# Kernel optimization log

Measured on AMD Instinct MI355X. Metric: run time of the kernel, lower is better.

The kernel has to match this reference:

```python
import jax, jax.numpy as jnp
import numpy as np

N = 100000
E = 1600000
C = 128
NEG_SLOPE = 0.2
BN_EPS = 1e-5


def setup_inputs() -> dict:
    key = jax.random.key(0)
    ks = jax.random.split(key, 6)
    x = jax.random.normal(ks[0], (N, C), dtype=jnp.float32)
    edge_index = jax.random.randint(ks[1], (2, E), 0, N, dtype=jnp.int64)
    # Glorot-ish scaled params, stacked over the 3 layers (all 128->128)
    Ws = jax.random.normal(ks[2], (3, C, C), dtype=jnp.float32) * (1.0 / np.sqrt(C))
    att_srcs = jax.random.normal(ks[3], (3, C), dtype=jnp.float32) * (1.0 / np.sqrt(C))
    att_dsts = jax.random.normal(ks[4], (3, C), dtype=jnp.float32) * (1.0 / np.sqrt(C))
    biases = jnp.zeros((3, C), dtype=jnp.float32)
    gammas = jnp.ones((3, C), dtype=jnp.float32)
    betas = jnp.zeros((3, C), dtype=jnp.float32)
    return {"x": x, "edge_index": edge_index, "Ws": Ws, "att_srcs": att_srcs,
            "att_dsts": att_dsts, "biases": biases, "gammas": gammas, "betas": betas}


def _gat_layer(x, W, a_src, a_dst, bias, src, dst):
    # linear transform: [N, C]
    h = x @ W
    # per-node attention logits
    s_src = h @ a_src  # [N]
    s_dst = h @ a_dst  # [N]
    # edge-wise gather + leaky relu scoring
    e = jax.nn.leaky_relu(s_src[src] + s_dst[dst], NEG_SLOPE)  # [E+N]
    # scatter-softmax over incoming edges of each target node
    m = jax.ops.segment_max(e, dst, num_segments=N)  # every node has a self-loop
    ex = jnp.exp(e - m[dst])
    denom = jax.ops.segment_sum(ex, dst, num_segments=N)
    alpha = ex / denom[dst]  # [E+N]
    # scatter-add aggregation of alpha-weighted source features
    out = jax.ops.segment_sum(alpha[:, None] * h[src], dst, num_segments=N)
    return out + bias


def _batch_norm(x, gamma, beta):
    mu = jnp.mean(x, axis=0)
    var = jnp.mean(jnp.square(x - mu), axis=0)
    return gamma * (x - mu) * jax.lax.rsqrt(var + BN_EPS) + beta


def reference(x, edge_index, Ws, att_srcs, att_dsts, biases, gammas, betas):
    # PyG GATConv adds self-loops by default
    loops = jnp.arange(N, dtype=edge_index.dtype)
    src = jnp.concatenate([edge_index[0], loops])
    dst = jnp.concatenate([edge_index[1], loops])
    outs = []
    for l in range(3):
        x = _gat_layer(x, Ws[l], att_srcs[l], att_dsts[l], biases[l], src, dst)
        x = jax.nn.relu(x)
        x = _batch_norm(x, gammas[l], betas[l])
        outs.append(x)
    # jump=True: concat all layer outputs -> [N, 3*C]
    return jnp.concatenate(outs, axis=-1)
```

## Files before the change

### kernel.cpp

```cpp
#include <hip/hip_runtime.h>
#include <math.h>

#define N_NODES 100000
#define N_EDGES 1600000
#define M_TOT   (N_EDGES + N_NODES)
#define C_DIM   128
#define NEG_SLOPE 0.2f
#define BN_EPS 1e-5f

#define NBUCK 8
#define BUCK_NODES 12500
#define BUCK_CAP 240000

#define KS2 72
#define BN_NB 256
#define SCAN_NB 98

typedef _Float16 f16x8 __attribute__((ext_vector_type(8)));
typedef float f32x4 __attribute__((ext_vector_type(4)));

static __device__ __forceinline__ unsigned short f2h(float f) {
    _Float16 h = (_Float16)f;
    unsigned short u;
    __builtin_memcpy(&u, &h, 2);
    return u;
}
static __device__ __forceinline__ float h2f(unsigned short u) {
    _Float16 h;
    __builtin_memcpy(&h, &u, 2);
    return (float)h;
}

__global__ void zero_i32(int* __restrict__ p, int n) {
    int i = blockIdx.x * blockDim.x + threadIdx.x;
    if (i < n) p[i] = 0;
}

__global__ __launch_bounds__(256) void bucket_edges(const int* __restrict__ ei,
                                                    int* __restrict__ bucket_next,
                                                    int2* __restrict__ buckets) {
    __shared__ int cnt[NBUCK];
    __shared__ int base[NBUCK];
    int tid = threadIdx.x;
    if (tid < NBUCK) cnt[tid] = 0;
    __syncthreads();
    int m = blockIdx.x * 256 + tid;
    int src = 0, dst = 0, p = 0, myoff = 0;
    bool valid = (m < M_TOT);
    if (valid) {
        if (m < N_EDGES) { src = ei[m]; dst = ei[N_EDGES + m]; }
        else             { src = m - N_EDGES; dst = src; }
        p = dst / BUCK_NODES;
        myoff = atomicAdd(&cnt[p], 1);
    }
    __syncthreads();
    if (tid < NBUCK) base[tid] = (cnt[tid] > 0) ? atomicAdd(&bucket_next[tid], cnt[tid]) : 0;
    __syncthreads();
    if (valid) {
        buckets[(size_t)p * BUCK_CAP + base[p] + myoff] = make_int2(src, dst);
    }
}

__global__ __launch_bounds__(256) void count_deg_b(const int2* __restrict__ buckets,
                                                   const int* __restrict__ bucket_next,
                                                   int* __restrict__ deg) {
    int p = blockIdx.x & 7;
    int chunk = blockIdx.x >> 3;
    int len = bucket_next[p];
    const int2* b = buckets + (size_t)p * BUCK_CAP;
    int stride = (gridDim.x >> 3) * 256;
    for (int i = chunk * 256 + threadIdx.x; i < len; i += stride) {
        atomicAdd(&deg[b[i].y], 1);
    }
}

__global__ __launch_bounds__(256) void scatter_b(const int2* __restrict__ buckets,
                                                 const int* __restrict__ bucket_next,
                                                 int* __restrict__ nextp,
                                                 int* __restrict__ csr_src) {
    int p = blockIdx.x & 7;
    int chunk = blockIdx.x >> 3;
    int len = bucket_next[p];
    const int2* b = buckets + (size_t)p * BUCK_CAP;
    int stride = (gridDim.x >> 3) * 256;
    for (int i = chunk * 256 + threadIdx.x; i < len; i += stride) {
        int2 e = b[i];
        int pos = atomicAdd(&nextp[e.y], 1);
        csr_src[pos] = e.x;
    }
}

__global__ __launch_bounds__(256) void block_sums(const int* __restrict__ deg,
                                                  int* __restrict__ partials) {
    __shared__ int lds[256];
    int base = blockIdx.x * 1024;
    int s = 0;
    for (int i = threadIdx.x; i < 1024; i += 256) {
        int idx = base + i;
        if (idx < N_NODES) s += deg[idx];
    }
    lds[threadIdx.x] = s;
    __syncthreads();
    for (int off = 128; off > 0; off >>= 1) {
        if (threadIdx.x < off) lds[threadIdx.x] += lds[threadIdx.x + off];
        __syncthreads();
    }
    if (threadIdx.x == 0) partials[blockIdx.x] = lds[0];
}

__global__ __launch_bounds__(128) void scan_partials(int* __restrict__ partials, int nb,
                                                     int* __restrict__ row_ptr) {
    __shared__ int lds[128];
    int tid = threadIdx.x;
    int v = (tid < nb) ? partials[tid] : 0;
    lds[tid] = v;
    __syncthreads();
    for (int off = 1; off < 128; off <<= 1) {
        int t = (tid >= off) ? lds[tid - off] : 0;
        __syncthreads();
        lds[tid] += t;
        __syncthreads();
    }
    if (tid < nb) partials[tid] = lds[tid] - v;
    if (tid == 0) row_ptr[N_NODES] = M_TOT;
}

__global__ __launch_bounds__(256) void scan_write(const int* __restrict__ deg,
                                                  const int* __restrict__ partials,
                                                  int* __restrict__ row_ptr,
                                                  int* __restrict__ nextp) {
    __shared__ int lds[256];
    int tid = threadIdx.x;
    int base = blockIdx.x * 1024;
    int i0 = base + tid * 4;
    int d[4];
#pragma unroll
    for (int t = 0; t < 4; ++t)
        d[t] = (i0 + t < N_NODES) ? deg[i0 + t] : 0;
    int tsum = d[0] + d[1] + d[2] + d[3];
    lds[tid] = tsum;
    __syncthreads();
    for (int off = 1; off < 256; off <<= 1) {
        int v = (tid >= off) ? lds[tid - off] : 0;
        __syncthreads();
        lds[tid] += v;
        __syncthreads();
    }
    int excl = lds[tid] - tsum;
    int run = partials[blockIdx.x] + excl;
#pragma unroll
    for (int t = 0; t < 4; ++t) {
        if (i0 + t < N_NODES) {
            row_ptr[i0 + t] = run;
            nextp[i0 + t]   = run;
            run += d[t];
        }
    }
}

__global__ __launch_bounds__(256, 3) void gemm_attn(
    const float* __restrict__ X, int ldx,
    const float* __restrict__ W,
    const float* __restrict__ a_src, const float* __restrict__ a_dst,
    unsigned short* __restrict__ Hh, float* __restrict__ Ssrc,
    float* __restrict__ Sdst) {
    __shared__ unsigned short Xs[128 * KS2];
    __shared__ unsigned short Wt[128 * KS2];
    int tid = threadIdx.x;
    int rbase = blockIdx.x * 128;

    int wave = tid >> 6;
    int lane = tid & 63;
    int q = lane >> 4;
    int l15 = lane & 15;
    int wrow = wave * 32;

    f32x4 acc[2][8] = {};

    for (int kb = 0; kb < 128; kb += 64) {
        __syncthreads();
        {
            int rl = tid >> 4;
            int cg = (tid & 15) * 4;
#pragma unroll
            for (int i = 0; i < 8; ++i) {
                int r = rl + i * 16;
                int row = rbase + r;
                if (row >= N_NODES) row = N_NODES - 1;
                float4 v = *(const float4*)&X[(size_t)row * ldx + kb + cg];
                ushort4 o;
                o.x = f2h(v.x); o.y = f2h(v.y); o.z = f2h(v.z); o.w = f2h(v.w);
                *(ushort4*)&Xs[r * KS2 + cg] = o;
            }
        }
        {
            int kl = tid >> 5;
            int n4 = (tid & 31) * 4;
#pragma unroll
            for (int i = 0; i < 8; ++i) {
                int kk = kl + i * 8;
                float4 v = *(const float4*)&W[(kb + kk) * 128 + n4];
                Wt[(n4 + 0) * KS2 + kk] = f2h(v.x);
                Wt[(n4 + 1) * KS2 + kk] = f2h(v.y);
                Wt[(n4 + 2) * KS2 + kk] = f2h(v.z);
                Wt[(n4 + 3) * KS2 + kk] = f2h(v.w);
            }
        }
        __syncthreads();
#pragma unroll
        for (int ks = 0; ks < 64; ks += 32) {
            int k0 = ks + q * 8;
            f16x8 a0 = *(f16x8*)&Xs[(wrow + l15) * KS2 + k0];
            f16x8 a1 = *(f16x8*)&Xs[(wrow + 16 + l15) * KS2 + k0];
#pragma unroll
            for (int c = 0; c < 8; ++c) {
                f16x8 b = *(f16x8*)&Wt[(c * 16 + l15) * KS2 + k0];
                acc[0][c] = __builtin_amdgcn_mfma_f32_16x16x32_f16(a0, b, acc[0][c], 0, 0, 0);
                acc[1][c] = __builtin_amdgcn_mfma_f32_16x16x32_f16(a1, b, acc[1][c], 0, 0, 0);
            }
        }
    }

    float avs[8], avd[8];
#pragma unroll
    for (int c = 0; c < 8; ++c) {
        avs[c] = a_src[c * 16 + l15];
        avd[c] = a_dst[c * 16 + l15];
    }
#pragma unroll
    for (int r = 0; r < 2; ++r) {
        float ps[4] = {0, 0, 0, 0}, pd[4] = {0, 0, 0, 0};
#pragma unroll
        for (int g = 0; g < 4; ++g) {
            int row = rbase + wrow + r * 16 + q * 4 + g;
            bool ok = (row < N_NODES);
#pragma unroll
            for (int c = 0; c < 8; ++c) {
                float h = acc[r][c][g];
                if (ok) Hh[(size_t)row * 128 + c * 16 + l15] = f2h(h);
                ps[g] = fmaf(h, avs[c], ps[g]);
                pd[g] = fmaf(h, avd[c], pd[g]);
            }
        }
#pragma unroll
        for (int g = 0; g < 4; ++g) {
#pragma unroll
            for (int off = 1; off < 16; off <<= 1) {
                ps[g] += __shfl_xor(ps[g], off, 64);
                pd[g] += __shfl_xor(pd[g], off, 64);
            }
        }
        if (l15 == 0) {
#pragma unroll
            for (int g = 0; g < 4; ++g) {
                int row = rbase + wrow + r * 16 + q * 4 + g;
                if (row < N_NODES) {
                    Ssrc[row] = ps[g];
                    Sdst[row] = pd[g];
                }
            }
        }
    }
}

__global__ __launch_bounds__(256) void aggregate(
    const unsigned short* __restrict__ Hh, const int* __restrict__ row_ptr,
    const int* __restrict__ csr_src,
    const float* __restrict__ Ssrc, const float* __restrict__ Sdst,
    const float* __restrict__ bias, float* __restrict__ Y) {
    int wave = threadIdx.x >> 6;
    int lane = threadIdx.x & 63;
    int g = lane >> 4;
    int l15 = lane & 15;
    int v = blockIdx.x * 4 + wave;
    int start = row_ptr[v];
    int end = row_ptr[v + 1];
    float sdv = Sdst[v];

    float sself = Ssrc[v] + sdv;
    float m = (sself > 0.0f) ? sself : NEG_SLOPE * sself;

    float acc[8] = {0, 0, 0, 0, 0, 0, 0, 0};
    float denom = 0.0f;

    int j = start;
    for (; j + 8 <= end; j += 8) {
        int u0 = csr_src[j + g];
        int u1 = csr_src[j + 4 + g];
        float ss0 = Ssrc[u0];
        float ss1 = Ssrc[u1];
        f16x8 h0 = *(const f16x8*)&Hh[(size_t)u0 * 128 + l15 * 8];
        f16x8 h1 = *(const f16x8*)&Hh[(size_t)u1 * 128 + l15 * 8];
        float s0 = ss0 + sdv; s0 = (s0 > 0.0f) ? s0 : NEG_SLOPE * s0;
        float s1 = ss1 + sdv; s1 = (s1 > 0.0f) ? s1 : NEG_SLOPE * s1;
        float w0 = __expf(s0 - m);
        float w1 = __expf(s1 - m);
        denom += w0 + w1;
#pragma unroll
        for (int i = 0; i < 8; ++i) acc[i] = fmaf(w0, (float)h0[i], acc[i]);
#pragma unroll
        for (int i = 0; i < 8; ++i) acc[i] = fmaf(w1, (float)h1[i], acc[i]);
    }
    for (; j < end; j += 4) {
        int je = j + g;
        bool ok = (je < end);
        int u = ok ? csr_src[je] : v;
        float s = Ssrc[u] + sdv; s = (s > 0.0f) ? s : NEG_SLOPE * s;
        float w = ok ? __expf(s - m) : 0.0f;
        f16x8 h = *(const f16x8*)&Hh[(size_t)u * 128 + l15 * 8];
        denom += w;
#pragma unroll
        for (int i = 0; i < 8; ++i) acc[i] = fmaf(w, (float)h[i], acc[i]);
    }

#pragma unroll
    for (int i = 0; i < 8; ++i) {
        acc[i] += __shfl_xor(acc[i], 16, 64);
        acc[i] += __shfl_xor(acc[i], 32, 64);
    }
    denom += __shfl_xor(denom, 16, 64);
    denom += __shfl_xor(denom, 32, 64);

    if (g == 0) {
        float inv = 1.0f / denom;
        float4 b0 = *(const float4*)&bias[l15 * 8];
        float4 b1 = *(const float4*)&bias[l15 * 8 + 4];
        float4 o0, o1;
        o0.x = fmaxf(fmaf(acc[0], inv, b0.x), 0.0f);
        o0.y = fmaxf(fmaf(acc[1], inv, b0.y), 0.0f);
        o0.z = fmaxf(fmaf(acc[2], inv, b0.z), 0.0f);
        o0.w = fmaxf(fmaf(acc[3], inv, b0.w), 0.0f);
        o1.x = fmaxf(fmaf(acc[4], inv, b1.x), 0.0f);
        o1.y = fmaxf(fmaf(acc[5], inv, b1.y), 0.0f);
        o1.z = fmaxf(fmaf(acc[6], inv, b1.z), 0.0f);
        o1.w = fmaxf(fmaf(acc[7], inv, b1.w), 0.0f);
        *(float4*)&Y[(size_t)v * 128 + l15 * 8] = o0;
        *(float4*)&Y[(size_t)v * 128 + l15 * 8 + 4] = o1;
    }
}

__global__ __launch_bounds__(256) void bn_stats(const float* __restrict__ Y,
                                                float* __restrict__ partial) {
    __shared__ float red[256 * 8];
    int tid = threadIdx.x;
    int rowlane = tid >> 5;
    int cg = tid & 31;
    float4 s = make_float4(0, 0, 0, 0);
    float4 qq = make_float4(0, 0, 0, 0);
    for (int i = blockIdx.x * 8 + rowlane; i < N_NODES; i += BN_NB * 8) {
        float4 v = *(const float4*)&Y[(size_t)i * 128 + cg * 4];
        s.x += v.x; s.y += v.y; s.z += v.z; s.w += v.w;
        qq.x = fmaf(v.x, v.x, qq.x);
        qq.y = fmaf(v.y, v.y, qq.y);
        qq.z = fmaf(v.z, v.z, qq.z);
        qq.w = fmaf(v.w, v.w, qq.w);
    }
    float* r = &red[tid * 8];
    r[0] = s.x; r[1] = s.y; r[2] = s.z; r[3] = s.w;
    r[4] = qq.x; r[5] = qq.y; r[6] = qq.z; r[7] = qq.w;
    __syncthreads();
    for (int off = 4; off > 0; off >>= 1) {
        if (rowlane < off) {
            float* o = &red[(tid + off * 32) * 8];
#pragma unroll
            for (int t = 0; t < 8; ++t) r[t] += o[t];
        }
        __syncthreads();
    }
    if (rowlane == 0) {
        *(float4*)&partial[(size_t)blockIdx.x * 256 + cg * 4] =
            make_float4(r[0], r[1], r[2], r[3]);
        *(float4*)&partial[(size_t)blockIdx.x * 256 + 128 + cg * 4] =
            make_float4(r[4], r[5], r[6], r[7]);
    }
}

__global__ __launch_bounds__(256) void bn_finalize(const float* __restrict__ partial,
                                                   const float* __restrict__ gamma,
                                                   const float* __restrict__ beta,
                                                   float* __restrict__ gb) {
    __shared__ float tot[256];
    int tid = threadIdx.x;
    float acc = 0.0f;
    for (int b = 0; b < BN_NB; ++b) acc += partial[(size_t)b * 256 + tid];
    tot[tid] = acc;
    __syncthreads();
    if (tid < 128) {
        const float invN = 1.0f / (float)N_NODES;
        float mu = tot[tid] * invN;
        float var = tot[128 + tid] * invN - mu * mu;
        float g = gamma[tid] * rsqrtf(var + BN_EPS);
        gb[tid] = g;
        gb[128 + tid] = beta[tid] - mu * g;
    }
}

__global__ __launch_bounds__(256) void bn_apply(const float* __restrict__ Y,
                                                const float* __restrict__ gb,
                                                float* __restrict__ out) {
    int idx = blockIdx.x * blockDim.x + threadIdx.x;
    if (idx >= N_NODES * 32) return;
    int row = idx >> 5;
    int c4 = (idx & 31) * 4;
    float4 v = *(const float4*)&Y[(size_t)row * 128 + c4];
    float4 g = *(const float4*)&gb[c4];
    float4 b = *(const float4*)&gb[128 + c4];
    v.x = fmaf(v.x, g.x, b.x);
    v.y = fmaf(v.y, g.y, b.y);
    v.z = fmaf(v.z, g.z, b.z);
    v.w = fmaf(v.w, g.w, b.w);
    *(float4*)&out[(size_t)row * 384 + c4] = v;
}

extern "C" void kernel_launch(void* const* d_in, const int* in_sizes, int n_in,
                              void* d_out, int out_size, void* d_ws, size_t ws_size,
                              hipStream_t stream) {
    const float* x      = (const float*)d_in[0];
    const int*   ei     = (const int*)d_in[1];
    const float* Wall   = (const float*)d_in[2];
    const float* asrcs  = (const float*)d_in[3];
    const float* adsts  = (const float*)d_in[4];
    const float* biases = (const float*)d_in[5];
    const float* gammas = (const float*)d_in[6];
    const float* betas  = (const float*)d_in[7];
    float* out = (float*)d_out;

    unsigned short* Hh = (unsigned short*)d_ws;
    float* Y       = (float*)(Hh + (size_t)N_NODES * 128);
    float* Ssrc    = Y + (size_t)N_NODES * 128;
    float* Sdst    = Ssrc + N_NODES;
    float* bnpart  = Sdst + N_NODES;
    float* gb      = bnpart + BN_NB * 256;
    int* deg       = (int*)(gb + 256);
    int* bucket_next = deg + N_NODES;
    int* row_ptr   = bucket_next + NBUCK;
    int* nextp     = row_ptr + (N_NODES + 1);
    int* partials  = nextp + N_NODES;
    int* csr_src   = partials + 128;
    int2* buckets  = (int2*)(csr_src + M_TOT + 2);

    const int ZERO_CNT = N_NODES + NBUCK;
    const int NB_EDGE = (M_TOT + 255) / 256;
    const int NB_PART = 2048;

    zero_i32<<<(ZERO_CNT + 255) / 256, 256, 0, stream>>>(deg, ZERO_CNT);
    bucket_edges<<<NB_EDGE, 256, 0, stream>>>(ei, bucket_next, buckets);
    count_deg_b<<<NB_PART, 256, 0, stream>>>(buckets, bucket_next, deg);
    block_sums<<<SCAN_NB, 256, 0, stream>>>(deg, partials);
    scan_partials<<<1, 128, 0, stream>>>(partials, SCAN_NB, row_ptr);
    scan_write<<<SCAN_NB, 256, 0, stream>>>(deg, partials, row_ptr, nextp);
    scatter_b<<<NB_PART, 256, 0, stream>>>(buckets, bucket_next, nextp, csr_src);

    for (int l = 0; l < 3; ++l) {
        const float* xin = (l == 0) ? x : (out + (size_t)(l - 1) * 128);
        int ldx = (l == 0) ? 128 : 384;
        gemm_attn<<<(N_NODES + 127) / 128, 256, 0, stream>>>(
            xin, ldx, Wall + (size_t)l * 128 * 128,
            asrcs + l * 128, adsts + l * 128, Hh, Ssrc, Sdst);
        aggregate<<<N_NODES / 4, 256, 0, stream>>>(
            Hh, row_ptr, csr_src, Ssrc, Sdst, biases + l * 128, Y);
        bn_stats<<<BN_NB, 256, 0, stream>>>(Y, bnpart);
        bn_finalize<<<1, 256, 0, stream>>>(bnpart, gammas + l * 128,
                                           betas + l * 128, gb);
        bn_apply<<<(N_NODES * 32 + 255) / 256, 256, 0, stream>>>(
            Y, gb, out + (size_t)l * 128);
    }
}
```

Before: 809.8 us.

## Fuse batch-norm apply into next layer GEMM load and unroll aggregation by 16

For layers after the first, the GEMM kernel reads the raw pre-BN activations Y, applies the BN scale/shift while staging into shared memory, and writes the normalized output into the concatenated result. This removes the separate bn_apply pass for the first two layers, saving one read and write of the feature matrix per layer. The aggregation kernel also gets a 16-edge unrolled loop to issue more independent gathers per iteration. The cost is higher register pressure in both kernels and extra global stores inside the GEMM.

```diff
diff --git a/kernel.cpp b/kernel.cpp
--- a/kernel.cpp
+++ b/kernel.cpp
@@ -162,6 +162,8 @@
     const float* __restrict__ X, int ldx,
     const float* __restrict__ W,
     const float* __restrict__ a_src, const float* __restrict__ a_dst,
+    const float* __restrict__ gbv,
+    float* __restrict__ outw,
     unsigned short* __restrict__ Hh, float* __restrict__ Ssrc,
     float* __restrict__ Sdst) {
     __shared__ unsigned short Xs[128 * KS2];
@@ -182,12 +184,26 @@
         {
             int rl = tid >> 4;
             int cg = (tid & 15) * 4;
+            float4 gg = make_float4(1.f, 1.f, 1.f, 1.f);
+            float4 bb = make_float4(0.f, 0.f, 0.f, 0.f);
+            if (gbv) {
+                gg = *(const float4*)&gbv[kb + cg];
+                bb = *(const float4*)&gbv[128 + kb + cg];
+            }
 #pragma unroll
             for (int i = 0; i < 8; ++i) {
                 int r = rl + i * 16;
-                int row = rbase + r;
-                if (row >= N_NODES) row = N_NODES - 1;
+                int row0 = rbase + r;
+                bool ok = (row0 < N_NODES);
+                int row = ok ? row0 : (N_NODES - 1);
                 float4 v = *(const float4*)&X[(size_t)row * ldx + kb + cg];
+                if (gbv) {
+                    v.x = fmaf(v.x, gg.x, bb.x);
+                    v.y = fmaf(v.y, gg.y, bb.y);
+                    v.z = fmaf(v.z, gg.z, bb.z);
+                    v.w = fmaf(v.w, gg.w, bb.w);
+                    if (ok) *(float4*)&outw[(size_t)row * 384 + kb + cg] = v;
+                }
                 ushort4 o;
                 o.x = f2h(v.x); o.y = f2h(v.y); o.z = f2h(v.z); o.w = f2h(v.w);
                 *(ushort4*)&Xs[r * KS2 + cg] = o;
@@ -284,6 +300,37 @@
     float denom = 0.0f;
 
     int j = start;
+    for (; j + 16 <= end; j += 16) {
+        int u0 = csr_src[j + g];
+        int u1 = csr_src[j + 4 + g];
+        int u2 = csr_src[j + 8 + g];
+        int u3 = csr_src[j + 12 + g];
+        float ss0 = Ssrc[u0];
+        float ss1 = Ssrc[u1];
+        float ss2 = Ssrc[u2];
+        float ss3 = Ssrc[u3];
+        f16x8 h0 = *(const f16x8*)&Hh[(size_t)u0 * 128 + l15 * 8];
+        f16x8 h1 = *(const f16x8*)&Hh[(size_t)u1 * 128 + l15 * 8];
+        f16x8 h2 = *(const f16x8*)&Hh[(size_t)u2 * 128 + l15 * 8];
+        f16x8 h3 = *(const f16x8*)&Hh[(size_t)u3 * 128 + l15 * 8];
+        float s0 = ss0 + sdv; s0 = (s0 > 0.0f) ? s0 : NEG_SLOPE * s0;
+        float s1 = ss1 + sdv; s1 = (s1 > 0.0f) ? s1 : NEG_SLOPE * s1;
+        float s2 = ss2 + sdv; s2 = (s2 > 0.0f) ? s2 : NEG_SLOPE * s2;
+        float s3 = ss3 + sdv; s3 = (s3 > 0.0f) ? s3 : NEG_SLOPE * s3;
+        float w0 = __expf(s0 - m);
+        float w1 = __expf(s1 - m);
+        float w2 = __expf(s2 - m);
+        float w3 = __expf(s3 - m);
+        denom += (w0 + w1) + (w2 + w3);
+#pragma unroll
+        for (int i = 0; i < 8; ++i) acc[i] = fmaf(w0, (float)h0[i], acc[i]);
+#pragma unroll
+        for (int i = 0; i < 8; ++i) acc[i] = fmaf(w1, (float)h1[i], acc[i]);
+#pragma unroll
+        for (int i = 0; i < 8; ++i) acc[i] = fmaf(w2, (float)h2[i], acc[i]);
+#pragma unroll
+        for (int i = 0; i < 8; ++i) acc[i] = fmaf(w3, (float)h3[i], acc[i]);
+    }
     for (; j + 8 <= end; j += 8) {
         int u0 = csr_src[j + g];
         int u1 = csr_src[j + 4 + g];
@@ -452,17 +499,21 @@
     scatter_b<<<NB_PART, 256, 0, stream>>>(buckets, bucket_next, nextp, csr_src);
 
     for (int l = 0; l < 3; ++l) {
-        const float* xin = (l == 0) ? x : (out + (size_t)(l - 1) * 128);
-        int ldx = (l == 0) ? 128 : 384;
+        const float* xin;
+        int ldx;
+        const float* gbl;
+        float* outw;
+        if (l == 0) { xin = x; ldx = 128; gbl = nullptr; outw = nullptr; }
+        else        { xin = Y; ldx = 128; gbl = gb; outw = out + (size_t)(l - 1) * 128; }
         gemm_attn<<<(N_NODES + 127) / 128, 256, 0, stream>>>(
             xin, ldx, Wall + (size_t)l * 128 * 128,
-            asrcs + l * 128, adsts + l * 128, Hh, Ssrc, Sdst);
+            asrcs + l * 128, adsts + l * 128, gbl, outw, Hh, Ssrc, Sdst);
         aggregate<<<N_NODES / 4, 256, 0, stream>>>(
             Hh, row_ptr, csr_src, Ssrc, Sdst, biases + l * 128, Y);
         bn_stats<<<BN_NB, 256, 0, stream>>>(Y, bnpart);
         bn_finalize<<<1, 256, 0, stream>>>(bnpart, gammas + l * 128,
                                            betas + l * 128, gb);
-        bn_apply<<<(N_NODES * 32 + 255) / 256, 256, 0, stream>>>(
-            Y, gb, out + (size_t)l * 128);
-    }
-}
+    }
+    bn_apply<<<(N_NODES * 32 + 255) / 256, 256, 0, stream>>>(
+        Y, gb, out + (size_t)2 * 128);
+}
```

After: 803.8 us. No clear change (-0.7%).
